# Kernel tuning notes

Hardware: AMD Instinct MI355X
Metric: run time of the kernel (lower is better)

Reference implementation:

```python
import jax, jax.numpy as jnp
import numpy as np

N_NODES = 50000
N_EDGES = 1600000
IN_DIM = 128
HIDDEN = 16
HEADS = 8
OUT_DIM = 64


def setup_inputs() -> dict:
    key = jax.random.key(0)
    k1, k2, k3, k4, k5 = jax.random.split(key, 5)
    h = jax.random.normal(k1, (N_NODES, IN_DIM), dtype=jnp.float32)
    W1 = jax.random.normal(k2, (IN_DIM, HEADS * HIDDEN), dtype=jnp.float32) * (IN_DIM ** -0.5)
    W2 = jax.random.normal(k3, (HEADS * HIDDEN, OUT_DIM), dtype=jnp.float32) * ((HEADS * HIDDEN) ** -0.5)
    src = jax.random.randint(k4, (N_EDGES,), 0, N_NODES, dtype=jnp.int32)
    dst = jax.random.randint(k5, (N_EDGES,), 0, N_NODES, dtype=jnp.int32)
    return {"h": h, "W1": W1, "W2": W2, "src": src, "dst": dst}


def dot_gat_conv(h, W, src, dst, num_heads, out_feats):
    # Project and split heads: [N, H, D]
    feat = (h @ W).reshape(-1, num_heads, out_feats)
    fs = feat[src]                       # [E, H, D] gather
    fd = feat[dst]                       # [E, H, D] gather
    scale = jnp.asarray(out_feats, feat.dtype) ** -0.5
    e = jnp.einsum('ehd,ehd->eh', fs, fd) * scale  # [E, H] scaled dot score
    # Edge softmax over incoming edges of each destination node
    m = jax.ops.segment_max(e, dst, num_segments=N_NODES)   # [N, H]
    m = jnp.where(jnp.isfinite(m), m, jnp.zeros_like(m))    # isolated nodes
    ex = jnp.exp(e - m[dst])                                 # [E, H]
    denom = jax.ops.segment_sum(ex, dst, num_segments=N_NODES)  # [N, H]
    a = ex / jnp.maximum(denom[dst], jnp.asarray(1e-9, ex.dtype))  # [E, H]
    # Weighted scatter-sum aggregation: [N, H, D]
    return jax.ops.segment_sum(a[:, :, None] * fs, dst, num_segments=N_NODES)


def reference(h, W1, W2, src, dst):
    h1 = dot_gat_conv(h, W1, src, dst, HEADS, HIDDEN)  # [N, H, hidden]
    h1 = jax.nn.elu(h1).reshape(N_NODES, HEADS * HIDDEN)  # flatten(1)
    # Dropout: eval-mode identity
    h2 = dot_gat_conv(h1, W2, src, dst, 1, OUT_DIM)  # [N, 1, out]
    return h2.mean(axis=1)  # [N, out]
```

## Files before the change

kernel.cpp:

```cpp
#include <hip/hip_runtime.h>
#include <hip/hip_bf16.h>

#define N_NODES 50000
#define N_EDGES 1600000
#define NBUCK 98
#define EPB 4096
#define NB_A ((N_EDGES + EPB - 1) / EPB)

typedef short bf16x8 __attribute__((ext_vector_type(8)));
typedef float f32x4  __attribute__((ext_vector_type(4)));
typedef float f32x2  __attribute__((ext_vector_type(2)));

__device__ __forceinline__ float bf16_raw_to_f32(unsigned short u) {
    return __uint_as_float(((unsigned)u) << 16);
}
__device__ __forceinline__ unsigned short f32_to_bf16_raw(float v) {
    unsigned u = __float_as_uint(v);
    return (unsigned short)((u + 0x7fffu + ((u >> 16) & 1u)) >> 16);
}
__device__ __forceinline__ float load_elem(const void* p, size_t i, int f) {
    if (f) return ((const float*)p)[i];
    return bf16_raw_to_f32(((const unsigned short*)p)[i]);
}
__device__ __forceinline__ void unpack8v(uint4 u, f32x2* f) {
    f[0] = (f32x2){__uint_as_float(u.x << 16), __uint_as_float(u.x & 0xffff0000u)};
    f[1] = (f32x2){__uint_as_float(u.y << 16), __uint_as_float(u.y & 0xffff0000u)};
    f[2] = (f32x2){__uint_as_float(u.z << 16), __uint_as_float(u.z & 0xffff0000u)};
    f[3] = (f32x2){__uint_as_float(u.w << 16), __uint_as_float(u.w & 0xffff0000u)};
}

__global__ void detect_dtype_kernel(const unsigned short* __restrict__ w1raw,
                                    int* __restrict__ flag, int* __restrict__ bcnt) {
    __shared__ float red[256];
    if (threadIdx.x < NBUCK) bcnt[threadIdx.x] = 0;
    float mx = 0.f;
    for (int i = threadIdx.x * 2; i < 16384; i += 512) {
        float v = fabsf(bf16_raw_to_f32(w1raw[i]));
        if (!isnan(v)) mx = fmaxf(mx, v);
    }
    red[threadIdx.x] = mx;
    __syncthreads();
    for (int s = 128; s > 0; s >>= 1) {
        if (threadIdx.x < s) red[threadIdx.x] = fmaxf(red[threadIdx.x], red[threadIdx.x + s]);
        __syncthreads();
    }
    if (threadIdx.x == 0) flag[0] = (red[0] > 1e4f) ? 1 : 0;
}

#define WPAD 136
__global__ void prep_kernel(const void* __restrict__ W1, const void* __restrict__ W2,
                            unsigned short* __restrict__ W1T,
                            unsigned short* __restrict__ W2T,
                            const int* __restrict__ flag) {
    const int f = *flag;
    int bid = blockIdx.x, tid = threadIdx.x;
    if (bid < 8) {
        int n = bid * 16 + (tid & 15);
        int kb = (tid >> 4) * 8;
        for (int j = 0; j < 8; ++j)
            W1T[n * WPAD + kb + j] = f32_to_bf16_raw(load_elem(W1, (size_t)(kb + j) * 128 + n, f));
    } else {
        int n = (bid - 8) * 16 + (tid & 15);
        int kb = (tid >> 4) * 8;
        for (int j = 0; j < 8; ++j)
            W2T[n * WPAD + kb + j] = f32_to_bf16_raw(load_elem(W2, (size_t)(kb + j) * 64 + n, f));
    }
}

__global__ void bucket_count_kernel(const int* __restrict__ dst,
                                    int* __restrict__ bcnt, int E) {
    __shared__ int hist[NBUCK];
    int t = threadIdx.x;
    if (t < NBUCK) hist[t] = 0;
    __syncthreads();
    int e0 = blockIdx.x * EPB;
    for (int k = 0; k < 16; ++k) {
        int e = e0 + k * 256 + t;
        if (e < E) atomicAdd(&hist[dst[e] >> 9], 1);
    }
    __syncthreads();
    if (t < NBUCK && hist[t]) atomicAdd(&bcnt[t], hist[t]);
}

__global__ void bucket_scan_kernel(const int* __restrict__ bcnt,
                                   int* __restrict__ bbase, int* __restrict__ bcur) {
    __shared__ int tmp[128];
    int t = threadIdx.x;
    int v = (t < NBUCK) ? bcnt[t] : 0;
    tmp[t] = v;
    __syncthreads();
    for (int off = 1; off < 128; off <<= 1) {
        int x = (t >= off) ? tmp[t - off] : 0;
        __syncthreads();
        tmp[t] += x;
        __syncthreads();
    }
    if (t < NBUCK) { int ex = tmp[t] - v; bbase[t] = ex; bcur[t] = ex; }
    if (t == NBUCK - 1) bbase[NBUCK] = tmp[t];
}

__global__ void binA_kernel(const int* __restrict__ src, const int* __restrict__ dst,
                            int* __restrict__ bcur, unsigned* __restrict__ inter, int E) {
    __shared__ int hist[NBUCK], gbase[NBUCK], cur[NBUCK];
    int t = threadIdx.x;
    if (t < NBUCK) hist[t] = 0;
    __syncthreads();
    int e0 = blockIdx.x * EPB;
    for (int k = 0; k < 16; ++k) {
        int e = e0 + k * 256 + t;
        if (e < E) atomicAdd(&hist[dst[e] >> 9], 1);
    }
    __syncthreads();
    if (t < NBUCK) {
        int hv = hist[t];
        gbase[t] = hv ? atomicAdd(&bcur[t], hv) : 0;
        cur[t] = 0;
    }
    __syncthreads();
    for (int k = 0; k < 16; ++k) {
        int e = e0 + k * 256 + t;
        if (e < E) {
            int d = dst[e];
            int b = d >> 9;
            int off = atomicAdd(&cur[b], 1);
            inter[gbase[b] + off] = (unsigned)src[e] | ((unsigned)(d & 511) << 16);
        }
    }
}

__global__ void binB_kernel(const unsigned* __restrict__ inter,
                            const int* __restrict__ bbase,
                            int* __restrict__ csr_src, int* __restrict__ start,
                            int N, int E) {
    int b = blockIdx.x;
    int node0 = b << 9;
    int lo = bbase[b], hi = bbase[b + 1];
    __shared__ int hist[512];
    __shared__ int t2[256];
    int t = threadIdx.x;
    hist[t] = 0; hist[t + 256] = 0;
    __syncthreads();
    for (int e = lo + t; e < hi; e += 256) atomicAdd(&hist[inter[e] >> 16], 1);
    __syncthreads();
    int s0 = hist[2 * t], s1 = hist[2 * t + 1];
    t2[t] = s0 + s1;
    __syncthreads();
    for (int off = 1; off < 256; off <<= 1) {
        int x = (t >= off) ? t2[t - off] : 0;
        __syncthreads();
        t2[t] += x;
        __syncthreads();
    }
    int base = (t == 0) ? 0 : t2[t - 1];
    hist[2 * t] = base;
    hist[2 * t + 1] = base + s0;
    __syncthreads();
    int nodeCnt = min(512, N - node0);
    for (int i = t; i < nodeCnt; i += 256) start[node0 + i] = lo + hist[i];
    if (b == NBUCK - 1 && t == 0) start[N] = E;
    __syncthreads();
    for (int e = lo + t; e < hi; e += 256) {
        unsigned u = inter[e];
        int slot = lo + atomicAdd(&hist[u >> 16], 1);
        csr_src[slot] = (int)(u & 0xffffu);
    }
}

__global__ void gemm1_mfma_kernel(const void* __restrict__ h,
                                  const unsigned short* __restrict__ W1T,
                                  unsigned short* __restrict__ feat1, int N,
                                  const int* __restrict__ flag) {
    const int f = *flag;
    int lane = threadIdx.x & 63;
    int rbase = blockIdx.x * 64 + (threadIdx.x >> 6) * 16;
    int arow = rbase + (lane & 15);
    int arowc = min(arow, N - 1);
    int kb0 = (lane >> 4) * 8;

    f32x4 acc[8];
#pragma unroll
    for (int t = 0; t < 8; ++t) acc[t] = (f32x4){0.f, 0.f, 0.f, 0.f};

#pragma unroll
    for (int ks = 0; ks < 4; ++ks) {
        int kb = ks * 32 + kb0;
        bf16x8 afrag;
        if (f == 0) {
            afrag = *(const bf16x8*)((const unsigned short*)h + (size_t)arowc * 128 + kb);
        } else {
            const float* hp = (const float*)h + (size_t)arowc * 128 + kb;
#pragma unroll
            for (int j = 0; j < 8; ++j) afrag[j] = (short)f32_to_bf16_raw(hp[j]);
        }
#pragma unroll
        for (int t = 0; t < 8; ++t) {
            int n = t * 16 + (lane & 15);
            bf16x8 bfrag = *(const bf16x8*)(W1T + n * WPAD + kb);
            acc[t] = __builtin_amdgcn_mfma_f32_16x16x32_bf16(afrag, bfrag, acc[t], 0, 0, 0);
        }
    }
    int orow0 = rbase + (lane >> 4) * 4;
    int col = lane & 15;
#pragma unroll
    for (int t = 0; t < 8; ++t)
#pragma unroll
        for (int r = 0; r < 4; ++r) {
            int row = orow0 + r;
            if (row < N)
                feat1[(size_t)row * 128 + t * 16 + col] = f32_to_bf16_raw(acc[t][r]);
        }
}

__global__ void gemm2_mfma_kernel(const unsigned short* __restrict__ agg1e,
                                  const unsigned short* __restrict__ W2T,
                                  unsigned short* __restrict__ feat2, int N) {
    int lane = threadIdx.x & 63;
    int rbase = blockIdx.x * 64 + (threadIdx.x >> 6) * 16;
    int arow = rbase + (lane & 15);
    int arowc = min(arow, N - 1);
    int kb0 = (lane >> 4) * 8;

    f32x4 acc[4];
#pragma unroll
    for (int t = 0; t < 4; ++t) acc[t] = (f32x4){0.f, 0.f, 0.f, 0.f};

#pragma unroll
    for (int ks = 0; ks < 4; ++ks) {
        int kb = ks * 32 + kb0;
        bf16x8 afrag = *(const bf16x8*)(agg1e + (size_t)arowc * 128 + kb);
#pragma unroll
        for (int t = 0; t < 4; ++t) {
            int n = t * 16 + (lane & 15);
            bf16x8 bfrag = *(const bf16x8*)(W2T + n * WPAD + kb);
            acc[t] = __builtin_amdgcn_mfma_f32_16x16x32_bf16(afrag, bfrag, acc[t], 0, 0, 0);
        }
    }
    int orow0 = rbase + (lane >> 4) * 4;
    int col = lane & 15;
#pragma unroll
    for (int t = 0; t < 4; ++t)
#pragma unroll
        for (int r = 0; r < 4; ++r) {
            int row = orow0 + r;
            if (row < N)
                feat2[(size_t)row * 64 + t * 16 + col] = f32_to_bf16_raw(acc[t][r]);
        }
}

__global__ void gat1_kernel(const unsigned short* __restrict__ feat1,
                            const int* __restrict__ csr_src,
                            const int* __restrict__ start,
                            unsigned short* __restrict__ agg1e, int N) {
    int wave = blockIdx.x * 4 + (threadIdx.x >> 6);
    int lane = threadIdx.x & 63;
    int g = lane >> 3, gl = lane & 7;
    int dstn = wave * 8 + g;
    if (dstn >= N) return;

    const char* fb = (const char*)feat1;
    unsigned loff = (unsigned)gl << 5;
    unsigned drow = ((unsigned)dstn << 8) + loff;
    f32x2 fd2[8];
    unpack8v(*(const uint4*)(fb + drow), fd2);
    unpack8v(*(const uint4*)(fb + drow + 16), fd2 + 4);

    float l = 0.f;
    f32x2 acc2[8];
#pragma unroll
    for (int k = 0; k < 8; ++k) acc2[k] = (f32x2){0.f, 0.f};

    int e0 = start[dstn], e1 = start[dstn + 1];
    int base = e0;
    for (; base + 2 <= e1; base += 2) {
        int s0 = csr_src[base], s1 = csr_src[base + 1];
        const char* r0 = fb + ((unsigned)s0 << 8) + loff;
        const char* r1 = fb + ((unsigned)s1 << 8) + loff;
        uint4 a0 = *(const uint4*)r0, a1 = *(const uint4*)(r0 + 16);
        uint4 b0 = *(const uint4*)r1, b1 = *(const uint4*)(r1 + 16);
        f32x2 f0[8], f1[8];
        unpack8v(a0, f0); unpack8v(a1, f0 + 4);
        unpack8v(b0, f1); unpack8v(b1, f1 + 4);
        f32x2 p0 = fd2[0] * f0[0];
        f32x2 p1 = fd2[0] * f1[0];
#pragma unroll
        for (int k = 1; k < 8; ++k) { p0 += fd2[k] * f0[k]; p1 += fd2[k] * f1[k]; }
        float q0 = p0.x + p0.y;
        float q1 = p1.x + p1.y;
        float w0 = __expf(q0 * 0.25f);
        float w1 = __expf(q1 * 0.25f);
        f32x2 W0 = (f32x2){w0, w0}, W1 = (f32x2){w1, w1};
#pragma unroll
        for (int k = 0; k < 8; ++k) {
            acc2[k] += W0 * f0[k];
            acc2[k] += W1 * f1[k];
        }
        l += w0 + w1;
    }
    if (base < e1) {
        int s = csr_src[base];
        const char* r0 = fb + ((unsigned)s << 8) + loff;
        uint4 a0 = *(const uint4*)r0, a1 = *(const uint4*)(r0 + 16);
        f32x2 fv[8];
        unpack8v(a0, fv); unpack8v(a1, fv + 4);
        f32x2 p = fd2[0] * fv[0];
#pragma unroll
        for (int k = 1; k < 8; ++k) p += fd2[k] * fv[k];
        float w = __expf((p.x + p.y) * 0.25f);
        f32x2 W = (f32x2){w, w};
#pragma unroll
        for (int k = 0; k < 8; ++k) acc2[k] += W * fv[k];
        l += w;
    }
    float rcp = 1.f / fmaxf(l, 1e-9f);
    unsigned pk[8];
#pragma unroll
    for (int k = 0; k < 8; ++k) {
        float x0 = acc2[k].x * rcp, x1 = acc2[k].y * rcp;
        x0 = (x0 > 0.f) ? x0 : expm1f(x0);
        x1 = (x1 > 0.f) ? x1 : expm1f(x1);
        pk[k] = (unsigned)f32_to_bf16_raw(x0) | ((unsigned)f32_to_bf16_raw(x1) << 16);
    }
    *(uint4*)((char*)agg1e + drow)      = (uint4){pk[0], pk[1], pk[2], pk[3]};
    *(uint4*)((char*)agg1e + drow + 16) = (uint4){pk[4], pk[5], pk[6], pk[7]};
}

__global__ void gat2_kernel(const unsigned short* __restrict__ feat2,
                            const int* __restrict__ csr_src,
                            const int* __restrict__ start,
                            void* __restrict__ out, int N,
                            const int* __restrict__ flag) {
    int wave = blockIdx.x * 4 + (threadIdx.x >> 6);
    int lane = threadIdx.x & 63;
    int g = lane >> 3, gl = lane & 7;
    int dstn = wave * 8 + g;
    if (dstn >= N) return;
    const int f = *flag;

    const char* fb = (const char*)feat2;
    unsigned loff = (unsigned)gl << 4;
    unsigned drow = ((unsigned)dstn << 7) + loff;
    f32x2 fd2[4];
    unpack8v(*(const uint4*)(fb + drow), fd2);

    float l = 0.f;
    f32x2 acc2[4];
#pragma unroll
    for (int k = 0; k < 4; ++k) acc2[k] = (f32x2){0.f, 0.f};

    int e0 = start[dstn], e1 = start[dstn + 1];
    int base = e0;
    for (; base + 2 <= e1; base += 2) {
        int s0 = csr_src[base], s1 = csr_src[base + 1];
        uint4 u0 = *(const uint4*)(fb + ((unsigned)s0 << 7) + loff);
        uint4 u1 = *(const uint4*)(fb + ((unsigned)s1 << 7) + loff);
        f32x2 f0[4], f1[4];
        unpack8v(u0, f0); unpack8v(u1, f1);
        f32x2 p0 = fd2[0] * f0[0];
        f32x2 p1 = fd2[0] * f1[0];
#pragma unroll
        for (int k = 1; k < 4; ++k) { p0 += fd2[k] * f0[k]; p1 += fd2[k] * f1[k]; }
        float q0 = p0.x + p0.y;
        float q1 = p1.x + p1.y;
        q0 += __shfl_xor(q0, 1); q1 += __shfl_xor(q1, 1);
        q0 += __shfl_xor(q0, 2); q1 += __shfl_xor(q1, 2);
        q0 += __shfl_xor(q0, 4); q1 += __shfl_xor(q1, 4);
        float w0 = __expf(q0 * 0.125f);
        float w1 = __expf(q1 * 0.125f);
        f32x2 W0 = (f32x2){w0, w0}, W1 = (f32x2){w1, w1};
#pragma unroll
        for (int k = 0; k < 4; ++k) {
            acc2[k] += W0 * f0[k];
            acc2[k] += W1 * f1[k];
        }
        l += w0 + w1;
    }
    if (base < e1) {
        int s = csr_src[base];
        uint4 u = *(const uint4*)(fb + ((unsigned)s << 7) + loff);
        f32x2 fv[4];
        unpack8v(u, fv);
        f32x2 p = fd2[0] * fv[0];
#pragma unroll
        for (int k = 1; k < 4; ++k) p += fd2[k] * fv[k];
        float q = p.x + p.y;
        q += __shfl_xor(q, 1);
        q += __shfl_xor(q, 2);
        q += __shfl_xor(q, 4);
        float w = __expf(q * 0.125f);
        f32x2 W = (f32x2){w, w};
#pragma unroll
        for (int k = 0; k < 4; ++k) acc2[k] += W * fv[k];
        l += w;
    }
    float rcp = 1.f / fmaxf(l, 1e-9f);
    float v[8];
#pragma unroll
    for (int k = 0; k < 4; ++k) {
        v[2 * k]     = acc2[k].x * rcp;
        v[2 * k + 1] = acc2[k].y * rcp;
    }
    if (f) {
        float* op = (float*)out + ((size_t)dstn << 6) + (gl << 3);
        *(float4*)(op)     = (float4){v[0], v[1], v[2], v[3]};
        *(float4*)(op + 4) = (float4){v[4], v[5], v[6], v[7]};
    } else {
        uint4 pk;
        pk.x = (unsigned)f32_to_bf16_raw(v[0]) | ((unsigned)f32_to_bf16_raw(v[1]) << 16);
        pk.y = (unsigned)f32_to_bf16_raw(v[2]) | ((unsigned)f32_to_bf16_raw(v[3]) << 16);
        pk.z = (unsigned)f32_to_bf16_raw(v[4]) | ((unsigned)f32_to_bf16_raw(v[5]) << 16);
        pk.w = (unsigned)f32_to_bf16_raw(v[6]) | ((unsigned)f32_to_bf16_raw(v[7]) << 16);
        *(uint4*)((unsigned short*)out + ((size_t)dstn << 6) + (gl << 3)) = pk;
    }
}

extern "C" void kernel_launch(void* const* d_in, const int* in_sizes, int n_in,
                              void* d_out, int out_size, void* d_ws, size_t ws_size,
                              hipStream_t stream) {
    const void* h  = d_in[0];
    const void* W1 = d_in[1];
    const void* W2 = d_in[2];
    const int* src = (const int*)d_in[3];
    const int* dst = (const int*)d_in[4];

    float* ws = (float*)d_ws;
    unsigned short* feat1 = (unsigned short*)ws;
    unsigned short* agg1e = (unsigned short*)(ws + 3200000);
    unsigned short* feat2 = (unsigned short*)ws;
    unsigned* inter       = (unsigned*)(ws + 6400000);
    int*   csr_src        = (int*)(ws + 9600000);
    int*   start          = (int*)(ws + 11200000);
    int*   flag           = (int*)(ws + 11330000);
    int*   bcnt           = (int*)(ws + 11331000);
    int*   bbase          = (int*)(ws + 11332000);
    int*   bcur           = (int*)(ws + 11333000);
    unsigned short* W1T   = (unsigned short*)(ws + 11340000);
    unsigned short* W2T   = (unsigned short*)(ws + 11350000);

    detect_dtype_kernel<<<1, 256, 0, stream>>>((const unsigned short*)W1, flag, bcnt);
    prep_kernel<<<12, 256, 0, stream>>>(W1, W2, W1T, W2T, flag);

    bucket_count_kernel<<<NB_A, 256, 0, stream>>>(dst, bcnt, N_EDGES);
    bucket_scan_kernel<<<1, 128, 0, stream>>>(bcnt, bbase, bcur);
    binA_kernel<<<NB_A, 256, 0, stream>>>(src, dst, bcur, inter, N_EDGES);
    binB_kernel<<<NBUCK, 256, 0, stream>>>(inter, bbase, csr_src, start, N_NODES, N_EDGES);

    gemm1_mfma_kernel<<<(N_NODES + 63) / 64, 256, 0, stream>>>(h, W1T, feat1, N_NODES, flag);
    int nwaves = (N_NODES + 7) / 8;
    gat1_kernel<<<(nwaves + 3) / 4, 256, 0, stream>>>(feat1, csr_src, start, agg1e, N_NODES);
    gemm2_mfma_kernel<<<(N_NODES + 63) / 64, 256, 0, stream>>>(agg1e, W2T, feat2, N_NODES);
    gat2_kernel<<<(nwaves + 3) / 4, 256, 0, stream>>>(feat2, csr_src, start, d_out, N_NODES, flag);
}
```

Measured before the change: 293.5 us.

## Assign one wave per destination node and split edges across lane groups

Both GAT aggregation kernels now use a full 64-lane wave for each destination node instead of one 8-lane group per node. The eight lane groups each take a different incoming edge, so 16 edges are handled per main-loop step and up to 8 per tail step, with masking. Partial sums and softmax denominators are then combined across groups with xor shuffles. This is meant to expose more memory-level parallelism on the gathers and shorten each wave's serial edge chain. In exchange it launches eight times as many waves and adds a cross-group reduction and idle lanes in the tail.

```diff
diff --git a/kernel.cpp b/kernel.cpp
--- a/kernel.cpp
+++ b/kernel.cpp
@@ -251,11 +251,10 @@
                             const int* __restrict__ csr_src,
                             const int* __restrict__ start,
                             unsigned short* __restrict__ agg1e, int N) {
-    int wave = blockIdx.x * 4 + (threadIdx.x >> 6);
+    int dstn = blockIdx.x * 4 + (threadIdx.x >> 6);
+    if (dstn >= N) return;
     int lane = threadIdx.x & 63;
     int g = lane >> 3, gl = lane & 7;
-    int dstn = wave * 8 + g;
-    if (dstn >= N) return;
 
     const char* fb = (const char*)feat1;
     unsigned loff = (unsigned)gl << 5;
@@ -271,8 +270,9 @@
 
     int e0 = start[dstn], e1 = start[dstn + 1];
     int base = e0;
-    for (; base + 2 <= e1; base += 2) {
-        int s0 = csr_src[base], s1 = csr_src[base + 1];
+    for (; base + 16 <= e1; base += 16) {
+        int s0 = csr_src[base + g];
+        int s1 = csr_src[base + 8 + g];
         const char* r0 = fb + ((unsigned)s0 << 8) + loff;
         const char* r1 = fb + ((unsigned)s1 << 8) + loff;
         uint4 a0 = *(const uint4*)r0, a1 = *(const uint4*)(r0 + 16);
@@ -284,10 +284,8 @@
         f32x2 p1 = fd2[0] * f1[0];
 #pragma unroll
         for (int k = 1; k < 8; ++k) { p0 += fd2[k] * f0[k]; p1 += fd2[k] * f1[k]; }
-        float q0 = p0.x + p0.y;
-        float q1 = p1.x + p1.y;
-        float w0 = __expf(q0 * 0.25f);
-        float w1 = __expf(q1 * 0.25f);
+        float w0 = __expf((p0.x + p0.y) * 0.25f);
+        float w1 = __expf((p1.x + p1.y) * 0.25f);
         f32x2 W0 = (f32x2){w0, w0}, W1 = (f32x2){w1, w1};
 #pragma unroll
         for (int k = 0; k < 8; ++k) {
@@ -296,8 +294,10 @@
         }
         l += w0 + w1;
     }
-    if (base < e1) {
-        int s = csr_src[base];
+    for (; base < e1; base += 8) {
+        int ed = base + g;
+        bool act = ed < e1;
+        int s = act ? csr_src[ed] : 0;
         const char* r0 = fb + ((unsigned)s << 8) + loff;
         uint4 a0 = *(const uint4*)r0, a1 = *(const uint4*)(r0 + 16);
         f32x2 fv[8];
@@ -305,23 +305,34 @@
         f32x2 p = fd2[0] * fv[0];
 #pragma unroll
         for (int k = 1; k < 8; ++k) p += fd2[k] * fv[k];
-        float w = __expf((p.x + p.y) * 0.25f);
+        float w = act ? __expf((p.x + p.y) * 0.25f) : 0.f;
         f32x2 W = (f32x2){w, w};
 #pragma unroll
         for (int k = 0; k < 8; ++k) acc2[k] += W * fv[k];
         l += w;
     }
-    float rcp = 1.f / fmaxf(l, 1e-9f);
-    unsigned pk[8];
-#pragma unroll
-    for (int k = 0; k < 8; ++k) {
-        float x0 = acc2[k].x * rcp, x1 = acc2[k].y * rcp;
-        x0 = (x0 > 0.f) ? x0 : expm1f(x0);
-        x1 = (x1 > 0.f) ? x1 : expm1f(x1);
-        pk[k] = (unsigned)f32_to_bf16_raw(x0) | ((unsigned)f32_to_bf16_raw(x1) << 16);
-    }
-    *(uint4*)((char*)agg1e + drow)      = (uint4){pk[0], pk[1], pk[2], pk[3]};
-    *(uint4*)((char*)agg1e + drow + 16) = (uint4){pk[4], pk[5], pk[6], pk[7]};
+#pragma unroll
+    for (int off = 8; off <= 32; off <<= 1) {
+        l += __shfl_xor(l, off);
+#pragma unroll
+        for (int k = 0; k < 8; ++k) {
+            acc2[k].x += __shfl_xor(acc2[k].x, off);
+            acc2[k].y += __shfl_xor(acc2[k].y, off);
+        }
+    }
+    if (g == 0) {
+        float rcp = 1.f / fmaxf(l, 1e-9f);
+        unsigned pk[8];
+#pragma unroll
+        for (int k = 0; k < 8; ++k) {
+            float x0 = acc2[k].x * rcp, x1 = acc2[k].y * rcp;
+            x0 = (x0 > 0.f) ? x0 : expm1f(x0);
+            x1 = (x1 > 0.f) ? x1 : expm1f(x1);
+            pk[k] = (unsigned)f32_to_bf16_raw(x0) | ((unsigned)f32_to_bf16_raw(x1) << 16);
+        }
+        *(uint4*)((char*)agg1e + drow)      = (uint4){pk[0], pk[1], pk[2], pk[3]};
+        *(uint4*)((char*)agg1e + drow + 16) = (uint4){pk[4], pk[5], pk[6], pk[7]};
+    }
 }
 
 __global__ void gat2_kernel(const unsigned short* __restrict__ feat2,
@@ -330,29 +341,27 @@
                             void* __restrict__ out, int N,
                             const int* __restrict__ flag) {
     int wave = blockIdx.x * 4 + (threadIdx.x >> 6);
+    if (wave >= N) return;
     int lane = threadIdx.x & 63;
-    int g = lane >> 3, gl = lane & 7;
-    int dstn = wave * 8 + g;
-    if (dstn >= N) return;
+    int grp = lane >> 3, gl = lane & 7;
     const int f = *flag;
-
     const char* fb = (const char*)feat2;
     unsigned loff = (unsigned)gl << 4;
-    unsigned drow = ((unsigned)dstn << 7) + loff;
     f32x2 fd2[4];
-    unpack8v(*(const uint4*)(fb + drow), fd2);
+    unpack8v(*(const uint4*)(fb + (((unsigned)wave << 7) + loff)), fd2);
 
     float l = 0.f;
     f32x2 acc2[4];
 #pragma unroll
     for (int k = 0; k < 4; ++k) acc2[k] = (f32x2){0.f, 0.f};
 
-    int e0 = start[dstn], e1 = start[dstn + 1];
+    int e0 = start[wave], e1 = start[wave + 1];
     int base = e0;
-    for (; base + 2 <= e1; base += 2) {
-        int s0 = csr_src[base], s1 = csr_src[base + 1];
-        uint4 u0 = *(const uint4*)(fb + ((unsigned)s0 << 7) + loff);
-        uint4 u1 = *(const uint4*)(fb + ((unsigned)s1 << 7) + loff);
+    for (; base + 16 <= e1; base += 16) {
+        int s0 = csr_src[base + grp];
+        int s1 = csr_src[base + 8 + grp];
+        uint4 u0 = *(const uint4*)(fb + (((unsigned)s0 << 7) + loff));
+        uint4 u1 = *(const uint4*)(fb + (((unsigned)s1 << 7) + loff));
         f32x2 f0[4], f1[4];
         unpack8v(u0, f0); unpack8v(u1, f1);
         f32x2 p0 = fd2[0] * f0[0];
@@ -374,9 +383,11 @@
         }
         l += w0 + w1;
     }
-    if (base < e1) {
-        int s = csr_src[base];
-        uint4 u = *(const uint4*)(fb + ((unsigned)s << 7) + loff);
+    for (; base < e1; base += 8) {
+        int ed = base + grp;
+        bool act = ed < e1;
+        int s = act ? csr_src[ed] : 0;
+        uint4 u = *(const uint4*)(fb + (((unsigned)s << 7) + loff));
         f32x2 fv[4];
         unpack8v(u, fv);
         f32x2 p = fd2[0] * fv[0];
@@ -386,30 +397,41 @@
         q += __shfl_xor(q, 1);
         q += __shfl_xor(q, 2);
         q += __shfl_xor(q, 4);
-        float w = __expf(q * 0.125f);
+        float w = act ? __expf(q * 0.125f) : 0.f;
         f32x2 W = (f32x2){w, w};
 #pragma unroll
         for (int k = 0; k < 4; ++k) acc2[k] += W * fv[k];
         l += w;
     }
-    float rcp = 1.f / fmaxf(l, 1e-9f);
-    float v[8];
-#pragma unroll
-    for (int k = 0; k < 4; ++k) {
-        v[2 * k]     = acc2[k].x * rcp;
-        v[2 * k + 1] = acc2[k].y * rcp;
-    }
-    if (f) {
-        float* op = (float*)out + ((size_t)dstn << 6) + (gl << 3);
-        *(float4*)(op)     = (float4){v[0], v[1], v[2], v[3]};
-        *(float4*)(op + 4) = (float4){v[4], v[5], v[6], v[7]};
-    } else {
-        uint4 pk;
-        pk.x = (unsigned)f32_to_bf16_raw(v[0]) | ((unsigned)f32_to_bf16_raw(v[1]) << 16);
-        pk.y = (unsigned)f32_to_bf16_raw(v[2]) | ((unsigned)f32_to_bf16_raw(v[3]) << 16);
-        pk.z = (unsigned)f32_to_bf16_raw(v[4]) | ((unsigned)f32_to_bf16_raw(v[5]) << 16);
-        pk.w = (unsigned)f32_to_bf16_raw(v[6]) | ((unsigned)f32_to_bf16_raw(v[7]) << 16);
-        *(uint4*)((unsigned short*)out + ((size_t)dstn << 6) + (gl << 3)) = pk;
+#pragma unroll
+    for (int off = 8; off <= 32; off <<= 1) {
+        l += __shfl_xor(l, off);
+#pragma unroll
+        for (int k = 0; k < 4; ++k) {
+            acc2[k].x += __shfl_xor(acc2[k].x, off);
+            acc2[k].y += __shfl_xor(acc2[k].y, off);
+        }
+    }
+    if (grp == 0) {
+        float rcp = 1.f / fmaxf(l, 1e-9f);
+        float v[8];
+#pragma unroll
+        for (int k = 0; k < 4; ++k) {
+            v[2 * k]     = acc2[k].x * rcp;
+            v[2 * k + 1] = acc2[k].y * rcp;
+        }
+        if (f) {
+            float* op = (float*)out + ((size_t)wave << 6) + (gl << 3);
+            *(float4*)(op)     = (float4){v[0], v[1], v[2], v[3]};
+            *(float4*)(op + 4) = (float4){v[4], v[5], v[6], v[7]};
+        } else {
+            uint4 pk;
+            pk.x = (unsigned)f32_to_bf16_raw(v[0]) | ((unsigned)f32_to_bf16_raw(v[1]) << 16);
+            pk.y = (unsigned)f32_to_bf16_raw(v[2]) | ((unsigned)f32_to_bf16_raw(v[3]) << 16);
+            pk.z = (unsigned)f32_to_bf16_raw(v[4]) | ((unsigned)f32_to_bf16_raw(v[5]) << 16);
+            pk.w = (unsigned)f32_to_bf16_raw(v[6]) | ((unsigned)f32_to_bf16_raw(v[7]) << 16);
+            *(uint4*)((unsigned short*)out + ((size_t)wave << 6) + (gl << 3)) = pk;
+        }
     }
 }
 
@@ -445,8 +467,7 @@
     binB_kernel<<<NBUCK, 256, 0, stream>>>(inter, bbase, csr_src, start, N_NODES, N_EDGES);
 
     gemm1_mfma_kernel<<<(N_NODES + 63) / 64, 256, 0, stream>>>(h, W1T, feat1, N_NODES, flag);
-    int nwaves = (N_NODES + 7) / 8;
-    gat1_kernel<<<(nwaves + 3) / 4, 256, 0, stream>>>(feat1, csr_src, start, agg1e, N_NODES);
+    gat1_kernel<<<(N_NODES + 3) / 4, 256, 0, stream>>>(feat1, csr_src, start, agg1e, N_NODES);
     gemm2_mfma_kernel<<<(N_NODES + 63) / 64, 256, 0, stream>>>(agg1e, W2T, feat2, N_NODES);
-    gat2_kernel<<<(nwaves + 3) / 4, 256, 0, stream>>>(feat2, csr_src, start, d_out, N_NODES, flag);
-}
+    gat2_kernel<<<(N_NODES + 3) / 4, 256, 0, stream>>>(feat2, csr_src, start, d_out, N_NODES, flag);
+}
```

Result: no change. 295.7 us (+0.7%).
